# Performance work log

Measured on AMD Instinct MI355X. Metric: run time of the kernel, lower is better.

Reference implementation:

```python
import jax, jax.numpy as jnp
import numpy as np

C = 32        # latent_channels
BCH = 6       # bottleneck_channels
H, W = 180, 320
N = H * W
B = 32


def _hilbert_walk(h, w):
    """Faithful port of FlattenDeflatten._hilbert_curve: Morton/Z-order bit
    interleave over (i, j), stable-sorted by key (ties broken by raster index).
    Returns flat raster indices in walk order."""
    i = np.arange(h, dtype=np.int64)[:, None]
    j = np.arange(w, dtype=np.int64)[None, :]
    z = np.zeros((h, w), dtype=np.int64)
    for bit in range(16):
        z |= ((i >> bit) & 1) << (2 * bit + 1)
        z |= ((j >> bit) & 1) << (2 * bit)
    # coords.sort() on (z, flat_idx) == stable argsort of z over raster order
    return np.argsort(z.ravel(), kind='stable')


def setup_inputs() -> dict:
    key = jax.random.key(0)
    ks = jax.random.split(key, 6)
    walk = _hilbert_walk(H, W)
    unwalk = np.zeros_like(walk)
    unwalk[walk] = np.arange(N)
    # torch Conv1d default init: U(-1/sqrt(fan_in), 1/sqrt(fan_in)), kernel=1
    bf = 1.0 / np.sqrt(C)
    bd = 1.0 / np.sqrt(BCH)
    return {
        "latent": jax.random.normal(ks[0], (B, C, H, W), dtype=jnp.float32),
        "w_flat": jax.random.uniform(ks[1], (BCH, C), jnp.float32, -bf, bf),
        "b_flat": jax.random.uniform(ks[2], (BCH,), jnp.float32, -bf, bf),
        "w_deflat": jax.random.uniform(ks[3], (C, BCH), jnp.float32, -bd, bd),
        "b_deflat": jax.random.uniform(ks[4], (C,), jnp.float32, -bd, bd),
        "spatial_embed": jax.random.normal(ks[5], (1, C, N), dtype=jnp.float32) * 0.02,
        "walk_idx": jnp.asarray(walk, dtype=jnp.int32),
        "unwalk_idx": jnp.asarray(unwalk, dtype=jnp.int32),
    }


def reference(latent, w_flat, b_flat, w_deflat, b_deflat, spatial_embed,
              walk_idx, unwalk_idx):
    Bb, Cc, Hh, Ww = latent.shape
    # flatten: serialize along walk order, then 1x1 conv (channel GEMM)
    seq = latent.reshape(Bb, Cc, Hh * Ww)[:, :, walk_idx]          # (B, C, N)
    flat = jnp.einsum('oc,bcn->bon', w_flat, seq) + b_flat[:, None]  # (B, BCH, N)
    # deflatten: 1x1 conv back, add positional embed, inverse permutation
    dseq = (jnp.einsum('co,bon->bcn', w_deflat, flat)
            + b_deflat[:, None] + spatial_embed)                    # (B, C, N)
    recon = dseq[:, :, unwalk_idx].reshape(Bb, Cc, Hh, Ww)
    return (recon, flat)
```

## Files before the change

kernel.cpp:

```cpp
#include <hip/hip_runtime.h>

#define CCH 32
#define BCH 6
#define HH  180
#define WW  320
#define NN  (HH*WW)
#define BATCH 32
#define RPC 8
#define CHUNKS ((HH + RPC - 1)/RPC)
#define THREADS 640

typedef float f32x2 __attribute__((ext_vector_type(2)));
typedef float f32x4 __attribute__((ext_vector_type(4)));

__global__ __launch_bounds__(256) void permute_se(
    const float* __restrict__ se, const int* __restrict__ unwalk,
    const float* __restrict__ b_deflat, float* __restrict__ se_r)
{
    const int p = (blockIdx.x * 256 + threadIdx.x) * 4;
    if (p >= NN) return;
    const int i  = p / WW;
    const int j  = p % WW;
    const int nb = unwalk[(i & ~1)*WW + j];
    const int n2 = nb + 2*(i & 1);
    #pragma unroll 8
    for (int c = 0; c < CCH; ++c) {
        const f32x2 a  = *reinterpret_cast<const f32x2*>(se + (size_t)c*NN + n2);
        const f32x2 b2 = *reinterpret_cast<const f32x2*>(se + (size_t)c*NN + n2 + 4);
        const float bd = b_deflat[c];
        f32x4 v; v.x = a.x + bd; v.y = a.y + bd; v.z = b2.x + bd; v.w = b2.y + bd;
        *reinterpret_cast<f32x4*>(se_r + (size_t)c*NN + p) = v;
    }
}

template<int SE_RASTER>
__global__ __launch_bounds__(THREADS) void fused_flatten_deflatten(
    const float* __restrict__ latent,
    const float* __restrict__ w_flat,
    const float* __restrict__ b_flat,
    const float* __restrict__ w_deflat,
    const float* __restrict__ b_deflat,
    const float* __restrict__ se,
    const int*   __restrict__ unwalk,
    float* __restrict__ recon,
    float* __restrict__ flat_out)
{
    __shared__ float s_wf[BCH*CCH];
    __shared__ float s_wd[CCH*BCH];
    __shared__ float s_bf[BCH];
    __shared__ float s_bd[CCH];

    const int t  = threadIdx.x;
    const int bx = blockIdx.x;
    const int r  = bx >> 5;
    const int b  = bx & 31;

    if (t < BCH*CCH) { s_wf[t] = w_flat[t]; s_wd[t] = w_deflat[t]; }
    if (t < BCH)     s_bf[t] = b_flat[t];
    if (t < CCH)     s_bd[t] = b_deflat[t];
    __syncthreads();

    const int i  = RPC*r + t/80;
    if (i >= HH) return;
    const int j  = 4*(t%80);
    const int p  = i*WW + j;

    const int nb = unwalk[(i & ~1)*WW + j];
    const int n2 = nb + 2*(i & 1);

    const float* latb   = latent + (size_t)b * (CCH*NN) + p;
    float*       reconb = recon  + (size_t)b * (CCH*NN) + p;

    float acc[BCH][4];
    #pragma unroll
    for (int o = 0; o < BCH; ++o) {
        const float bo = s_bf[o];
        acc[o][0] = bo; acc[o][1] = bo; acc[o][2] = bo; acc[o][3] = bo;
    }

    #pragma unroll 8
    for (int c = 0; c < CCH; ++c) {
        const f32x4 x = __builtin_nontemporal_load(
            reinterpret_cast<const f32x4*>(latb + (size_t)c*NN));
        #pragma unroll
        for (int o = 0; o < BCH; ++o) {
            const float w = s_wf[o*CCH + c];
            acc[o][0] += w*x.x; acc[o][1] += w*x.y;
            acc[o][2] += w*x.z; acc[o][3] += w*x.w;
        }
    }

    float* fb = flat_out + (size_t)b * (BCH*NN) + n2;
    #pragma unroll
    for (int o = 0; o < BCH; ++o) {
        f32x2 lo; lo.x = acc[o][0]; lo.y = acc[o][1];
        f32x2 hi; hi.x = acc[o][2]; hi.y = acc[o][3];
        *reinterpret_cast<f32x2*>(fb + (size_t)o*NN)     = lo;
        *reinterpret_cast<f32x2*>(fb + (size_t)o*NN + 4) = hi;
    }

    #pragma unroll 8
    for (int c = 0; c < CCH; ++c) {
        float y0, y1, y2, y3;
        if (SE_RASTER) {
            const f32x4 s4 = *reinterpret_cast<const f32x4*>(se + (size_t)c*NN + p);
            y0 = s4.x; y1 = s4.y; y2 = s4.z; y3 = s4.w;
        } else {
            const f32x2 a  = *reinterpret_cast<const f32x2*>(se + (size_t)c*NN + n2);
            const f32x2 bq = *reinterpret_cast<const f32x2*>(se + (size_t)c*NN + n2 + 4);
            const float bd = s_bd[c];
            y0 = bd + a.x; y1 = bd + a.y; y2 = bd + bq.x; y3 = bd + bq.y;
        }
        #pragma unroll
        for (int o = 0; o < BCH; ++o) {
            const float w = s_wd[c*BCH + o];
            y0 += w*acc[o][0]; y1 += w*acc[o][1];
            y2 += w*acc[o][2]; y3 += w*acc[o][3];
        }
        f32x4 yv; yv.x = y0; yv.y = y1; yv.z = y2; yv.w = y3;
        __builtin_nontemporal_store(yv,
            reinterpret_cast<f32x4*>(reconb + (size_t)c*NN));
    }
}

extern "C" void kernel_launch(void* const* d_in, const int* in_sizes, int n_in,
                              void* d_out, int out_size, void* d_ws, size_t ws_size,
                              hipStream_t stream) {
    const float* latent   = (const float*)d_in[0];
    const float* w_flat   = (const float*)d_in[1];
    const float* b_flat   = (const float*)d_in[2];
    const float* w_deflat = (const float*)d_in[3];
    const float* b_deflat = (const float*)d_in[4];
    const float* se       = (const float*)d_in[5];
    const int*   unwalk   = (const int*)d_in[7];

    float* recon = (float*)d_out;
    float* flat  = (float*)d_out + (size_t)BATCH * CCH * NN;

    const size_t se_bytes = (size_t)CCH * NN * sizeof(float);
    dim3 grid(CHUNKS * BATCH);
    dim3 block(THREADS);

    if (ws_size >= se_bytes) {
        float* se_r = (float*)d_ws;
        permute_se<<<dim3((NN/4 + 255)/256), dim3(256), 0, stream>>>(
            se, unwalk, b_deflat, se_r);
        fused_flatten_deflatten<1><<<grid, block, 0, stream>>>(
            latent, w_flat, b_flat, w_deflat, b_deflat, se_r, unwalk, recon, flat);
    } else {
        fused_flatten_deflatten<0><<<grid, block, 0, stream>>>(
            latent, w_flat, b_flat, w_deflat, b_deflat, se, unwalk, recon, flat);
    }
}
```

Baseline: 131.7 us.

## Split fused flatten/deflatten into separate kernels and parallelize SE permute over channels

Replaces the single fused kernel with a flatten kernel that writes the bottleneck tensor and a deflatten kernel that reads it back to produce the reconstruction. The SE permute kernel is also spread across four channel groups via a second grid dimension. The intent is lower register pressure and better occupancy per kernel, at the cost of an extra round trip of the flat tensor through memory and an extra launch.

```diff
diff --git a/kernel.cpp b/kernel.cpp
--- a/kernel.cpp
+++ b/kernel.cpp
@@ -23,8 +23,10 @@
     const int j  = p % WW;
     const int nb = unwalk[(i & ~1)*WW + j];
     const int n2 = nb + 2*(i & 1);
-    #pragma unroll 8
-    for (int c = 0; c < CCH; ++c) {
+    const int c0 = blockIdx.y * (CCH/4);
+    #pragma unroll
+    for (int cc = 0; cc < CCH/4; ++cc) {
+        const int c = c0 + cc;
         const f32x2 a  = *reinterpret_cast<const f32x2*>(se + (size_t)c*NN + n2);
         const f32x2 b2 = *reinterpret_cast<const f32x2*>(se + (size_t)c*NN + n2 + 4);
         const float bd = b_deflat[c];
@@ -33,30 +35,73 @@
     }
 }
 
-template<int SE_RASTER>
-__global__ __launch_bounds__(THREADS) void fused_flatten_deflatten(
-    const float* __restrict__ latent,
-    const float* __restrict__ w_flat,
-    const float* __restrict__ b_flat,
-    const float* __restrict__ w_deflat,
-    const float* __restrict__ b_deflat,
-    const float* __restrict__ se,
-    const int*   __restrict__ unwalk,
-    float* __restrict__ recon,
+__global__ __launch_bounds__(THREADS) void flatten_k(
+    const float* __restrict__ latent, const float* __restrict__ w_flat,
+    const float* __restrict__ b_flat, const int* __restrict__ unwalk,
     float* __restrict__ flat_out)
 {
     __shared__ float s_wf[BCH*CCH];
-    __shared__ float s_wd[CCH*BCH];
     __shared__ float s_bf[BCH];
-    __shared__ float s_bd[CCH];
-
     const int t  = threadIdx.x;
     const int bx = blockIdx.x;
     const int r  = bx >> 5;
     const int b  = bx & 31;
 
-    if (t < BCH*CCH) { s_wf[t] = w_flat[t]; s_wd[t] = w_deflat[t]; }
+    if (t < BCH*CCH) s_wf[t] = w_flat[t];
     if (t < BCH)     s_bf[t] = b_flat[t];
+    __syncthreads();
+
+    const int i  = RPC*r + t/80;
+    if (i >= HH) return;
+    const int j  = 4*(t%80);
+    const int p  = i*WW + j;
+
+    const int nb = unwalk[(i & ~1)*WW + j];
+    const int n2 = nb + 2*(i & 1);
+
+    const float* latb = latent + (size_t)b * (CCH*NN) + p;
+
+    float acc[BCH][4];
+    #pragma unroll
+    for (int o = 0; o < BCH; ++o) {
+        const float bo = s_bf[o];
+        acc[o][0] = bo; acc[o][1] = bo; acc[o][2] = bo; acc[o][3] = bo;
+    }
+    #pragma unroll 8
+    for (int c = 0; c < CCH; ++c) {
+        const f32x4 x = __builtin_nontemporal_load(
+            reinterpret_cast<const f32x4*>(latb + (size_t)c*NN));
+        #pragma unroll
+        for (int o = 0; o < BCH; ++o) {
+            const float w = s_wf[o*CCH + c];
+            acc[o][0] += w*x.x; acc[o][1] += w*x.y;
+            acc[o][2] += w*x.z; acc[o][3] += w*x.w;
+        }
+    }
+    float* fb = flat_out + (size_t)b * (BCH*NN) + n2;
+    #pragma unroll
+    for (int o = 0; o < BCH; ++o) {
+        f32x2 lo; lo.x = acc[o][0]; lo.y = acc[o][1];
+        f32x2 hi; hi.x = acc[o][2]; hi.y = acc[o][3];
+        *reinterpret_cast<f32x2*>(fb + (size_t)o*NN)     = lo;
+        *reinterpret_cast<f32x2*>(fb + (size_t)o*NN + 4) = hi;
+    }
+}
+
+template<int SE_RASTER>
+__global__ __launch_bounds__(THREADS) void deflatten_k(
+    const float* __restrict__ flat_in, const float* __restrict__ w_deflat,
+    const float* __restrict__ b_deflat, const float* __restrict__ se,
+    const int* __restrict__ unwalk, float* __restrict__ recon)
+{
+    __shared__ float s_wd[CCH*BCH];
+    __shared__ float s_bd[CCH];
+    const int t  = threadIdx.x;
+    const int bx = blockIdx.x;
+    const int r  = bx >> 5;
+    const int b  = bx & 31;
+
+    if (t < BCH*CCH) s_wd[t] = w_deflat[t];
     if (t < CCH)     s_bd[t] = b_deflat[t];
     __syncthreads();
 
@@ -68,37 +113,16 @@
     const int nb = unwalk[(i & ~1)*WW + j];
     const int n2 = nb + 2*(i & 1);
 
-    const float* latb   = latent + (size_t)b * (CCH*NN) + p;
-    float*       reconb = recon  + (size_t)b * (CCH*NN) + p;
-
-    float acc[BCH][4];
+    float fv[BCH][4];
+    const float* fb = flat_in + (size_t)b * (BCH*NN) + n2;
     #pragma unroll
     for (int o = 0; o < BCH; ++o) {
-        const float bo = s_bf[o];
-        acc[o][0] = bo; acc[o][1] = bo; acc[o][2] = bo; acc[o][3] = bo;
+        const f32x2 lo = *reinterpret_cast<const f32x2*>(fb + (size_t)o*NN);
+        const f32x2 hi = *reinterpret_cast<const f32x2*>(fb + (size_t)o*NN + 4);
+        fv[o][0] = lo.x; fv[o][1] = lo.y; fv[o][2] = hi.x; fv[o][3] = hi.y;
     }
 
-    #pragma unroll 8
-    for (int c = 0; c < CCH; ++c) {
-        const f32x4 x = __builtin_nontemporal_load(
-            reinterpret_cast<const f32x4*>(latb + (size_t)c*NN));
-        #pragma unroll
-        for (int o = 0; o < BCH; ++o) {
-            const float w = s_wf[o*CCH + c];
-            acc[o][0] += w*x.x; acc[o][1] += w*x.y;
-            acc[o][2] += w*x.z; acc[o][3] += w*x.w;
-        }
-    }
-
-    float* fb = flat_out + (size_t)b * (BCH*NN) + n2;
-    #pragma unroll
-    for (int o = 0; o < BCH; ++o) {
-        f32x2 lo; lo.x = acc[o][0]; lo.y = acc[o][1];
-        f32x2 hi; hi.x = acc[o][2]; hi.y = acc[o][3];
-        *reinterpret_cast<f32x2*>(fb + (size_t)o*NN)     = lo;
-        *reinterpret_cast<f32x2*>(fb + (size_t)o*NN + 4) = hi;
-    }
-
+    float* reconb = recon + (size_t)b * (CCH*NN) + p;
     #pragma unroll 8
     for (int c = 0; c < CCH; ++c) {
         float y0, y1, y2, y3;
@@ -114,8 +138,8 @@
         #pragma unroll
         for (int o = 0; o < BCH; ++o) {
             const float w = s_wd[c*BCH + o];
-            y0 += w*acc[o][0]; y1 += w*acc[o][1];
-            y2 += w*acc[o][2]; y3 += w*acc[o][3];
+            y0 += w*fv[o][0]; y1 += w*fv[o][1];
+            y2 += w*fv[o][2]; y3 += w*fv[o][3];
         }
         f32x4 yv; yv.x = y0; yv.y = y1; yv.z = y2; yv.w = y3;
         __builtin_nontemporal_store(yv,
@@ -143,12 +167,14 @@
 
     if (ws_size >= se_bytes) {
         float* se_r = (float*)d_ws;
-        permute_se<<<dim3((NN/4 + 255)/256), dim3(256), 0, stream>>>(
+        permute_se<<<dim3((NN/4 + 255)/256, 4), dim3(256), 0, stream>>>(
             se, unwalk, b_deflat, se_r);
-        fused_flatten_deflatten<1><<<grid, block, 0, stream>>>(
-            latent, w_flat, b_flat, w_deflat, b_deflat, se_r, unwalk, recon, flat);
+        flatten_k<<<grid, block, 0, stream>>>(latent, w_flat, b_flat, unwalk, flat);
+        deflatten_k<1><<<grid, block, 0, stream>>>(flat, w_deflat, b_deflat,
+                                                   se_r, unwalk, recon);
     } else {
-        fused_flatten_deflatten<0><<<grid, block, 0, stream>>>(
-            latent, w_flat, b_flat, w_deflat, b_deflat, se, unwalk, recon, flat);
+        flatten_k<<<grid, block, 0, stream>>>(latent, w_flat, b_flat, unwalk, flat);
+        deflatten_k<0><<<grid, block, 0, stream>>>(flat, w_deflat, b_deflat,
+                                                   se, unwalk, recon);
     }
 }
```

Result: no change. 133.6 us (+1.4%).
